# Kernel optimization log

Hardware: AMD Instinct MI355X
Metric: run time of the kernel (lower is better)

The kernel has to match this reference:

```python
import jax, jax.numpy as jnp
import numpy as np

B, N, D = 4, 1024, 512
H = 8
HD = D // H  # 64
EPS = 1e-12  # F.normalize eps


def _l2_normalize(t):
    # torch.nn.functional.normalize(p=2, dim=-1): x / max(||x||_2, eps)
    nrm = jnp.sqrt(jnp.sum(t * t, axis=-1, keepdims=True))
    return t / jnp.maximum(nrm, EPS)


def setup_inputs() -> dict:
    key = jax.random.key(0)
    ks = jax.random.split(key, 5)
    scale = 1.0 / np.sqrt(D)
    inp = {
        "x": jax.random.normal(ks[0], (B, N, D), dtype=jnp.float32),
        "Wq": jax.random.normal(ks[1], (D, D), dtype=jnp.float32) * scale,
        "Wk": jax.random.normal(ks[2], (D, D), dtype=jnp.float32) * scale,
        "Wv": jax.random.normal(ks[3], (D, D), dtype=jnp.float32) * scale,
        "Wo": jax.random.normal(ks[4], (D, D), dtype=jnp.float32) * scale,
        "bq": jnp.zeros((D,), dtype=jnp.float32),
        "bk": jnp.zeros((D,), dtype=jnp.float32),
        "bv": jnp.zeros((D,), dtype=jnp.float32),
        "bo": jnp.zeros((D,), dtype=jnp.float32),
    }
    return inp


def reference(x, Wq, Wk, Wv, Wo, bq, bk, bv, bo):
    b, n, d = x.shape
    # projections (nn.Linear: x @ W.T + b), split heads -> (b, h, n, hd)
    def split_heads(t):
        return t.reshape(b, n, H, HD).transpose(0, 2, 1, 3)

    q = split_heads(x @ Wq.T + bq)
    k = split_heads(x @ Wk.T + bk)
    v = split_heads(x @ Wv.T + bv)

    q = _l2_normalize(jax.nn.elu(q))
    k = _l2_normalize(jax.nn.elu(k))

    # causal linear attention: running prefix sum of k (outer) v states
    kv_step = jnp.einsum('bhnd,bhne->bhnde', k, v)      # (b,h,n,hd,hd)
    kv_prefix = jnp.cumsum(kv_step, axis=2)             # causal prefix state
    out = jnp.einsum('bhnd,bhnde->bhne', q, kv_prefix)  # (b,h,n,hd)

    out = out.transpose(0, 2, 1, 3).reshape(b, n, d)
    return out @ Wo.T + bo
```

## Files before the change

### kernel.cpp

```cpp
#include <hip/hip_runtime.h>
#include <cmath>

#define BB 4
#define NN 1024
#define DD 512
#define HH 8
#define HDIM 64
#define ROWS (BB * NN)
#define NCHUNK 16
#define KA 512
#define WMAT ((size_t)512 * 512)

typedef _Float16 f16;
typedef f16   f16x8 __attribute__((ext_vector_type(8)));
typedef f16   f16x4 __attribute__((ext_vector_type(4)));
typedef float f32x4 __attribute__((ext_vector_type(4)));

#define GLOAD_LDS16(g, l) \
    __builtin_amdgcn_global_load_lds((const __attribute__((address_space(1))) void*)(g), \
                                     (__attribute__((address_space(3))) void*)(l), 16, 0, 0)

__global__ __launch_bounds__(256)
void split_all(const float* __restrict__ x,
               const float* __restrict__ Wq, const float* __restrict__ Wk,
               const float* __restrict__ Wv, const float* __restrict__ Wo,
               f16* __restrict__ xa, f16* __restrict__ wa)
{
    for (int f4 = blockIdx.x * 256 + threadIdx.x; f4 < 786432; f4 += 768 * 256) {
        const float* src;
        f16* dstbase;
        int t;
        if (f4 < 524288) {
            t = f4;
            src = x;
            dstbase = xa;
        } else {
            int w = f4 - 524288;
            int m = w >> 16;
            t = w & 65535;
            src = (m == 0) ? Wq : (m == 1) ? Wk : (m == 2) ? Wv : Wo;
            dstbase = wa + (size_t)m * WMAT;
        }
        float4 v = ((const float4*)src)[t];
        int r = t >> 7;
        int c = (t & 127) * 4;
        f16x4 h;
        h[0] = (f16)v.x; h[1] = (f16)v.y; h[2] = (f16)v.z; h[3] = (f16)v.w;
        *(f16x4*)(dstbase + (size_t)r * 512 + c) = h;
    }
}

template<int OUTMODE>
__global__ __launch_bounds__(256)
void mm_f16(const f16* __restrict__ A, const f16* __restrict__ Wm,
            const float* __restrict__ b0, const float* __restrict__ b1,
            const float* __restrict__ b2,
            f16* __restrict__ qf, f16* __restrict__ kf,
            f16* __restrict__ ktb, f16* __restrict__ vtb,
            float* __restrict__ obase)
{
    constexpr int BN = (OUTMODE == 0) ? 128 : 64;
    constexpr int NW = BN / 32;
    constexpr int BR = BN / 32;

    __shared__ __align__(16) f16 As[2][128 * 64];
    __shared__ __align__(16) f16 Bs[2][BN * 64];

    const int t    = threadIdx.x;
    const int lane = t & 63;
    const int wid  = t >> 6;
    const int wr   = wid >> 1;
    const int wc   = wid & 1;
    const int l16  = lane & 15;
    const int g16  = lane >> 4;

    const int nwg = 32 * gridDim.y;
    const int lin = blockIdx.y * 32 + blockIdx.x;
    const int swz = (lin & 7) * (nwg >> 3) + (lin >> 3);
    const int bx  = swz & 31;
    const int by  = swz >> 5;

    const int r0 = bx * 128;
    const int c0 = by * BN;
    const int z  = (OUTMODE == 0) ? (c0 >> 9) : 0;
    const int cw = (OUTMODE == 0) ? (c0 & 511) : c0;

    const f16* Wz = Wm + (size_t)z * WMAT;

    auto stage = [&](int buf, int kt) {
        const int kb = kt * 64;
        #pragma unroll
        for (int i = 0; i < 4; ++i) {
            int f = i * 256 + t;
            int row = f >> 3;
            int sc  = (f & 7) ^ (row & 7);
            GLOAD_LDS16(A + (size_t)(r0 + row) * KA + kb + sc * 8, As[buf] + f * 8);
        }
        #pragma unroll
        for (int i = 0; i < BR; ++i) {
            int f = i * 256 + t;
            int row = f >> 3;
            int sc  = (f & 7) ^ (row & 7);
            GLOAD_LDS16(Wz + (size_t)(cw + row) * KA + kb + sc * 8, Bs[buf] + f * 8);
        }
    };

    f32x4 acc[4][NW] = {};

    stage(0, 0);

    for (int kt = 0; kt < 8; ++kt) {
        const int buf = kt & 1;
        if (kt < 7) {
            stage(buf ^ 1, kt + 1);
            if (OUTMODE == 0) asm volatile("s_waitcnt vmcnt(8)" ::: "memory");
            else              asm volatile("s_waitcnt vmcnt(6)" ::: "memory");
        } else {
            asm volatile("s_waitcnt vmcnt(0)" ::: "memory");
        }
        __builtin_amdgcn_s_barrier();
        __builtin_amdgcn_sched_barrier(0);

        #pragma unroll
        for (int kk = 0; kk < 2; ++kk) {
            f16x8 af[4], bfr[NW];
            #pragma unroll
            for (int mi = 0; mi < 4; ++mi) {
                int lr = wr * 64 + mi * 16 + l16;
                int sc = (kk * 4 + g16) ^ (lr & 7);
                af[mi] = *(const f16x8*)(As[buf] + lr * 64 + sc * 8);
            }
            #pragma unroll
            for (int ni = 0; ni < NW; ++ni) {
                int lr = wc * (BN / 2) + ni * 16 + l16;
                int sc = (kk * 4 + g16) ^ (lr & 7);
                bfr[ni] = *(const f16x8*)(Bs[buf] + lr * 64 + sc * 8);
            }
            #pragma unroll
            for (int mi = 0; mi < 4; ++mi)
                #pragma unroll
                for (int ni = 0; ni < NW; ++ni)
                    acc[mi][ni] = __builtin_amdgcn_mfma_f32_16x16x32_f16(af[mi], bfr[ni], acc[mi][ni], 0, 0, 0);
        }
        __builtin_amdgcn_s_barrier();
    }

    if (OUTMODE == 1) {
        #pragma unroll
        for (int mi = 0; mi < 4; ++mi)
            #pragma unroll
            for (int ni = 0; ni < NW; ++ni) {
                int cg = c0 + wc * (BN / 2) + ni * 16 + l16;
                float bv = b0[cg];
                #pragma unroll
                for (int r = 0; r < 4; ++r) {
                    int rg = r0 + wr * 64 + mi * 16 + g16 * 4 + r;
                    obase[(size_t)rg * DD + cg] = acc[mi][ni][r] + bv;
                }
            }
    } else {
        const float* bias = (z == 0) ? b0 : (z == 1) ? b1 : b2;

        #pragma unroll
        for (int mi = 0; mi < 4; ++mi)
            #pragma unroll
            for (int ni = 0; ni < NW; ++ni) {
                float bv = bias[cw + wc * 64 + ni * 16 + l16];
                #pragma unroll
                for (int r = 0; r < 4; ++r) {
                    float v = acc[mi][ni][r] + bv;
                    if (z < 2) v = (v > 0.f) ? v : expm1f(v);
                    acc[mi][ni][r] = v;
                }
            }
        if (z < 2) {
            #pragma unroll
            for (int mi = 0; mi < 4; ++mi)
                #pragma unroll
                for (int r = 0; r < 4; ++r) {
                    float ss = 0.f;
                    #pragma unroll
                    for (int ni = 0; ni < NW; ++ni) ss += acc[mi][ni][r] * acc[mi][ni][r];
                    ss += __shfl_xor(ss, 1);
                    ss += __shfl_xor(ss, 2);
                    ss += __shfl_xor(ss, 4);
                    ss += __shfl_xor(ss, 8);
                    float sc = 1.f / fmaxf(sqrtf(ss), 1e-12f);
                    #pragma unroll
                    for (int ni = 0; ni < NW; ++ni) acc[mi][ni][r] *= sc;
                }
        }

        const int h = (cw >> 6) + wc;
        const int b = r0 >> 10;

        if (z <= 1) {
            f16* plane = (z == 0) ? qf : kf;
            #pragma unroll
            for (int mi = 0; mi < 4; ++mi)
                #pragma unroll
                for (int r = 0; r < 4; ++r) {
                    int rg = r0 + wr * 64 + mi * 16 + g16 * 4 + r;
                    f16* dst = plane + ((size_t)(b * HH + h) * NN + (rg & 1023)) * HDIM;
                    #pragma unroll
                    for (int ni = 0; ni < NW; ++ni) dst[ni * 16 + l16] = (f16)acc[mi][ni][r];
                }
        }

        if (z >= 1) {
            f16* tb = (z == 1) ? ktb : vtb;
            f16* T = (wid < 2) ? (As[0] + wid * 4096) : (Bs[0] + (wid - 2) * 4096);
            #pragma unroll
            for (int mi = 0; mi < 4; ++mi)
                #pragma unroll
                for (int ni = 0; ni < NW; ++ni)
                    #pragma unroll
                    for (int r = 0; r < 4; ++r) {
                        int n_ = mi * 16 + g16 * 4 + r;
                        int d_ = ni * 16 + l16;
                        *(f16*)((char*)T + d_ * 128 + (((n_ >> 3) ^ (d_ & 7)) * 16) + (n_ & 7) * 2)
                            = (f16)acc[mi][ni][r];
                    }
            __syncthreads();
            const int n0 = (r0 & 1023) + wr * 64;
            #pragma unroll
            for (int p = 0; p < 8; ++p) {
                int d_ = p * 8 + (lane >> 3);
                int ck = lane & 7;
                f16x8 v8 = *(const f16x8*)((char*)T + d_ * 128 + ((ck ^ (d_ & 7)) * 16));
                *(f16x8*)(tb + ((size_t)(b * HH + h) * HDIM + d_) * NN + n0 + ck * 8) = v8;
            }
        }
    }
}

__global__ __launch_bounds__(256)
void state_prefix(const f16* __restrict__ ktb, const f16* __restrict__ vtb,
                  f16* __restrict__ ptb)
{
    __shared__ __align__(16) f16 Kt[2][64 * 64];
    __shared__ __align__(16) f16 Vt[2][64 * 64];
    __shared__ __align__(16) f16 PtL[16 * 64];

    const int bh = blockIdx.x;
    const int eq = blockIdx.y;
    const int t  = threadIdx.x;
    const int lane = t & 63;
    const int wid  = t >> 6;
    const int l16  = lane & 15;
    const int g16  = lane >> 4;

    auto stage = [&](int ch, int buf) {
        #pragma unroll
        for (int i = 0; i < 2; ++i) {
            int f = i * 256 + t;
            int row = f >> 3;
            int sc  = (f & 7) ^ (row & 7);
            GLOAD_LDS16(ktb + ((size_t)bh * HDIM + row) * NN + ch * 64 + sc * 8, Kt[buf] + f * 8);
            GLOAD_LDS16(vtb + ((size_t)bh * HDIM + row) * NN + ch * 64 + sc * 8, Vt[buf] + f * 8);
        }
    };

    float pref[4] = {};
    const int d = wid * 16 + l16;

    stage(0, 0);

    for (int ch = 0; ch < NCHUNK; ++ch) {
        const int buf = ch & 1;
        stage(ch < 15 ? ch + 1 : 15, buf ^ 1);

        #pragma unroll
        for (int r = 0; r < 4; ++r) {
            int e = g16 * 4 + r;
            *(f16*)((char*)PtL + e * 128 + (((d >> 3) ^ (e & 7)) * 16) + (d & 7) * 2)
                = (f16)pref[r];
        }

        asm volatile("s_waitcnt vmcnt(4)" ::: "memory");
        asm volatile("s_waitcnt lgkmcnt(0)" ::: "memory");
        __builtin_amdgcn_s_barrier();
        __builtin_amdgcn_sched_barrier(0);

        {
            f16x4 v4 = *(const f16x4*)(PtL + t * 4);
            *(f16x4*)(ptb + (size_t)(bh * NCHUNK + ch) * 4096 + eq * 1024 + t * 4) = v4;
        }

        f32x4 sacc = {};
        #pragma unroll
        for (int ks = 0; ks < 2; ++ks) {
            int ra = eq * 16 + l16;
            f16x8 av = *(const f16x8*)(Vt[buf] + ra * 64 + ((ks * 4 + g16) ^ (ra & 7)) * 8);
            int rb = wid * 16 + l16;
            f16x8 bv = *(const f16x8*)(Kt[buf] + rb * 64 + ((ks * 4 + g16) ^ (rb & 7)) * 8);
            sacc = __builtin_amdgcn_mfma_f32_16x16x32_f16(av, bv, sacc, 0, 0, 0);
        }
        #pragma unroll
        for (int r = 0; r < 4; ++r) pref[r] += sacc[r];

        __builtin_amdgcn_s_barrier();
    }
}

__global__ __launch_bounds__(256)
void attn_chunk(const f16* __restrict__ qf, const f16* __restrict__ kf,
                const f16* __restrict__ vtb, const f16* __restrict__ ptb,
                f16* __restrict__ aug)
{
    __shared__ __align__(16) f16 Qs[64 * 64];
    __shared__ __align__(16) f16 Ks[64 * 64];
    __shared__ __align__(16) f16 Vt[64 * 64];
    __shared__ __align__(16) f16 Pt[64 * 64];
    __shared__ __align__(16) f16 Ss[64 * 64];

    const int bh = blockIdx.x;
    const int ch = blockIdx.y;
    const int t  = threadIdx.x;
    const int lane = t & 63;
    const int wid  = t >> 6;
    const int wr   = wid >> 1;
    const int wc   = wid & 1;
    const int l16  = lane & 15;
    const int g16  = lane >> 4;

    #pragma unroll
    for (int i = 0; i < 2; ++i) {
        int f = i * 256 + t;
        int row = f >> 3;
        int sc  = (f & 7) ^ (row & 7);
        GLOAD_LDS16(qf  + ((size_t)bh * NN + ch * 64 + row) * HDIM + sc * 8, Qs + f * 8);
        GLOAD_LDS16(kf  + ((size_t)bh * NN + ch * 64 + row) * HDIM + sc * 8, Ks + f * 8);
        GLOAD_LDS16(vtb + ((size_t)bh * HDIM + row) * NN + ch * 64 + sc * 8, Vt + f * 8);
        GLOAD_LDS16(ptb + (size_t)(bh * NCHUNK + ch) * 4096 + f * 8, Pt + f * 8);
    }
    __syncthreads();

    f32x4 sacc[2][2] = {};
    #pragma unroll
    for (int ks = 0; ks < 2; ++ks) {
        f16x8 af[2], bfr[2];
        #pragma unroll
        for (int mi = 0; mi < 2; ++mi) {
            int row = wr * 32 + mi * 16 + l16;
            int sc  = (ks * 4 + g16) ^ (row & 7);
            af[mi] = *(const f16x8*)(Qs + row * 64 + sc * 8);
        }
        #pragma unroll
        for (int ni = 0; ni < 2; ++ni) {
            int row = wc * 32 + ni * 16 + l16;
            int sc  = (ks * 4 + g16) ^ (row & 7);
            bfr[ni] = *(const f16x8*)(Ks + row * 64 + sc * 8);
        }
        #pragma unroll
        for (int mi = 0; mi < 2; ++mi)
            #pragma unroll
            for (int ni = 0; ni < 2; ++ni)
                sacc[mi][ni] = __builtin_amdgcn_mfma_f32_16x16x32_f16(af[mi], bfr[ni], sacc[mi][ni], 0, 0, 0);
    }
    #pragma unroll
    for (int mi = 0; mi < 2; ++mi)
        #pragma unroll
        for (int ni = 0; ni < 2; ++ni)
            #pragma unroll
            for (int r = 0; r < 4; ++r) {
                int i = wr * 32 + mi * 16 + g16 * 4 + r;
                int j = wc * 32 + ni * 16 + l16;
                float v = (j <= i) ? sacc[mi][ni][r] : 0.f;
                *(f16*)((char*)Ss + i * 128 + (((j >> 3) ^ (i & 7)) * 16) + (j & 7) * 2) = (f16)v;
            }
    __syncthreads();

    f32x4 oacc[2][2] = {};
    #pragma unroll
    for (int ks = 0; ks < 2; ++ks) {
        f16x8 af[2], bfr[2];
        #pragma unroll
        for (int mi = 0; mi < 2; ++mi) {
            int row = wr * 32 + mi * 16 + l16;
            int sc  = (ks * 4 + g16) ^ (row & 7);
            af[mi] = *(const f16x8*)(Qs + row * 64 + sc * 8);
        }
        #pragma unroll
        for (int ni = 0; ni < 2; ++ni) {
            int row = wc * 32 + ni * 16 + l16;
            int sc  = (ks * 4 + g16) ^ (row & 7);
            bfr[ni] = *(const f16x8*)(Pt + row * 64 + sc * 8);
        }
        #pragma unroll
        for (int mi = 0; mi < 2; ++mi)
            #pragma unroll
            for (int ni = 0; ni < 2; ++ni)
                oacc[mi][ni] = __builtin_amdgcn_mfma_f32_16x16x32_f16(af[mi], bfr[ni], oacc[mi][ni], 0, 0, 0);
    }
    #pragma unroll
    for (int ks = 0; ks < 2; ++ks) {
        f16x8 af[2], bfr[2];
        #pragma unroll
        for (int mi = 0; mi < 2; ++mi) {
            int row = wr * 32 + mi * 16 + l16;
            int sc  = (ks * 4 + g16) ^ (row & 7);
            af[mi] = *(const f16x8*)(Ss + row * 64 + sc * 8);
        }
        #pragma unroll
        for (int ni = 0; ni < 2; ++ni) {
            int row = wc * 32 + ni * 16 + l16;
            int sc  = (ks * 4 + g16) ^ (row & 7);
            bfr[ni] = *(const f16x8*)(Vt + row * 64 + sc * 8);
        }
        #pragma unroll
        for (int mi = 0; mi < 2; ++mi)
            #pragma unroll
            for (int ni = 0; ni < 2; ++ni)
                oacc[mi][ni] = __builtin_amdgcn_mfma_f32_16x16x32_f16(af[mi], bfr[ni], oacc[mi][ni], 0, 0, 0);
    }

    const int b = bh >> 3;
    const int h = bh & 7;
    #pragma unroll
    for (int mi = 0; mi < 2; ++mi)
        #pragma unroll
        for (int ni = 0; ni < 2; ++ni)
            #pragma unroll
            for (int r = 0; r < 4; ++r) {
                int i = wr * 32 + mi * 16 + g16 * 4 + r;
                int e = wc * 32 + ni * 16 + l16;
                aug[((size_t)(b * NN + ch * 64 + i)) * KA + h * HDIM + e] = (f16)oacc[mi][ni][r];
            }
}

extern "C" void kernel_launch(void* const* d_in, const int* in_sizes, int n_in,
                              void* d_out, int out_size, void* d_ws, size_t ws_size,
                              hipStream_t stream)
{
    (void)in_sizes; (void)n_in; (void)out_size; (void)ws_size;

    const float* x  = (const float*)d_in[0];
    const float* Wq = (const float*)d_in[1];
    const float* Wk = (const float*)d_in[2];
    const float* Wv = (const float*)d_in[3];
    const float* Wo = (const float*)d_in[4];
    const float* bq = (const float*)d_in[5];
    const float* bk = (const float*)d_in[6];
    const float* bv = (const float*)d_in[7];
    const float* bo = (const float*)d_in[8];
    float* out = (float*)d_out;

    char* ws = (char*)d_ws;
    f16* qf  = (f16*)(ws);
    f16* kf  = (f16*)(ws + (size_t)4  * 1024 * 1024);
    f16* ktb = (f16*)(ws + (size_t)8  * 1024 * 1024);
    f16* vtb = (f16*)(ws + (size_t)12 * 1024 * 1024);
    f16* ptb = (f16*)(ws + (size_t)16 * 1024 * 1024);
    f16* xa  = (f16*)(ws + (size_t)20 * 1024 * 1024);
    f16* aug = (f16*)(ws + (size_t)24 * 1024 * 1024);
    f16* wa  = (f16*)(ws + (size_t)28 * 1024 * 1024);

    dim3 blk(256);

    split_all<<<dim3(768), blk, 0, stream>>>(x, Wq, Wk, Wv, Wo, xa, wa);

    mm_f16<0><<<dim3(32, 12), blk, 0, stream>>>(xa, wa, bq, bk, bv, qf, kf, ktb, vtb, nullptr);

    state_prefix<<<dim3(32, 4), blk, 0, stream>>>(ktb, vtb, ptb);
    attn_chunk<<<dim3(32, NCHUNK), blk, 0, stream>>>(qf, kf, vtb, ptb, aug);

    mm_f16<1><<<dim3(32, 8), blk, 0, stream>>>(aug, wa + (size_t)3 * WMAT, bo, nullptr, nullptr,
                                               nullptr, nullptr, nullptr, nullptr, out);
}
```

Measured before the change: 56.07 us.

## Split QKV projection and overlap Q projection with K/V state prefix kernel

The fused QKV projection is split into a K/V-only projection kernel and a combined kernel whose first 128 blocks compute the Q projection while the remaining 128 blocks run the chunked KV-state prefix scan. The Q work is independent of the prefix scan, so running both in one launch fills the device better than the small 128-block state_prefix launch did on its own. The shared GEMM body is factored into a device function using one flat LDS buffer, and the output projection becomes its own kernel. The cost is a heterogeneous kernel whose LDS footprint is sized for the GEMM path, which may limit occupancy for the prefix blocks, and the prefix blocks can become the critical path.

Result: slower. 61.16 us (+9.1%).

```diff
diff --git a/kernel.cpp b/kernel.cpp
--- a/kernel.cpp
+++ b/kernel.cpp
@@ -50,21 +50,16 @@
     }
 }
 
-template<int OUTMODE>
-__global__ __launch_bounds__(256)
-void mm_f16(const f16* __restrict__ A, const f16* __restrict__ Wm,
-            const float* __restrict__ b0, const float* __restrict__ b1,
-            const float* __restrict__ b2,
-            f16* __restrict__ qf, f16* __restrict__ kf,
-            f16* __restrict__ ktb, f16* __restrict__ vtb,
-            float* __restrict__ obase)
-{
-    constexpr int BN = (OUTMODE == 0) ? 128 : 64;
-    constexpr int NW = BN / 32;
-    constexpr int BR = BN / 32;
-
-    __shared__ __align__(16) f16 As[2][128 * 64];
-    __shared__ __align__(16) f16 Bs[2][BN * 64];
+__device__ __forceinline__
+void proj_body(const f16* __restrict__ A, const f16* __restrict__ Wz,
+               const float* __restrict__ bias, const int z,
+               const int r0, const int cw,
+               f16* __restrict__ qf, f16* __restrict__ kf,
+               f16* __restrict__ ktb, f16* __restrict__ vtb,
+               f16* lds)
+{
+    f16* As0 = lds;
+    f16* Bs0 = lds + 16384;
 
     const int t    = threadIdx.x;
     const int lane = t & 63;
@@ -74,19 +69,6 @@
     const int l16  = lane & 15;
     const int g16  = lane >> 4;
 
-    const int nwg = 32 * gridDim.y;
-    const int lin = blockIdx.y * 32 + blockIdx.x;
-    const int swz = (lin & 7) * (nwg >> 3) + (lin >> 3);
-    const int bx  = swz & 31;
-    const int by  = swz >> 5;
-
-    const int r0 = bx * 128;
-    const int c0 = by * BN;
-    const int z  = (OUTMODE == 0) ? (c0 >> 9) : 0;
-    const int cw = (OUTMODE == 0) ? (c0 & 511) : c0;
-
-    const f16* Wz = Wm + (size_t)z * WMAT;
-
     auto stage = [&](int buf, int kt) {
         const int kb = kt * 64;
         #pragma unroll
@@ -94,18 +76,18 @@
             int f = i * 256 + t;
             int row = f >> 3;
             int sc  = (f & 7) ^ (row & 7);
-            GLOAD_LDS16(A + (size_t)(r0 + row) * KA + kb + sc * 8, As[buf] + f * 8);
-        }
-        #pragma unroll
-        for (int i = 0; i < BR; ++i) {
+            GLOAD_LDS16(A + (size_t)(r0 + row) * KA + kb + sc * 8, As0 + buf * 8192 + f * 8);
+        }
+        #pragma unroll
+        for (int i = 0; i < 4; ++i) {
             int f = i * 256 + t;
             int row = f >> 3;
             int sc  = (f & 7) ^ (row & 7);
-            GLOAD_LDS16(Wz + (size_t)(cw + row) * KA + kb + sc * 8, Bs[buf] + f * 8);
+            GLOAD_LDS16(Wz + (size_t)(cw + row) * KA + kb + sc * 8, Bs0 + buf * 8192 + f * 8);
         }
     };
 
-    f32x4 acc[4][NW] = {};
+    f32x4 acc[4][4] = {};
 
     stage(0, 0);
 
@@ -113,8 +95,7 @@
         const int buf = kt & 1;
         if (kt < 7) {
             stage(buf ^ 1, kt + 1);
-            if (OUTMODE == 0) asm volatile("s_waitcnt vmcnt(8)" ::: "memory");
-            else              asm volatile("s_waitcnt vmcnt(6)" ::: "memory");
+            asm volatile("s_waitcnt vmcnt(8)" ::: "memory");
         } else {
             asm volatile("s_waitcnt vmcnt(0)" ::: "memory");
         }
@@ -123,141 +104,161 @@
 
         #pragma unroll
         for (int kk = 0; kk < 2; ++kk) {
-            f16x8 af[4], bfr[NW];
+            f16x8 af[4], bfr[4];
             #pragma unroll
             for (int mi = 0; mi < 4; ++mi) {
                 int lr = wr * 64 + mi * 16 + l16;
                 int sc = (kk * 4 + g16) ^ (lr & 7);
-                af[mi] = *(const f16x8*)(As[buf] + lr * 64 + sc * 8);
-            }
-            #pragma unroll
-            for (int ni = 0; ni < NW; ++ni) {
-                int lr = wc * (BN / 2) + ni * 16 + l16;
+                af[mi] = *(const f16x8*)(As0 + buf * 8192 + lr * 64 + sc * 8);
+            }
+            #pragma unroll
+            for (int ni = 0; ni < 4; ++ni) {
+                int lr = wc * 64 + ni * 16 + l16;
                 int sc = (kk * 4 + g16) ^ (lr & 7);
-                bfr[ni] = *(const f16x8*)(Bs[buf] + lr * 64 + sc * 8);
+                bfr[ni] = *(const f16x8*)(Bs0 + buf * 8192 + lr * 64 + sc * 8);
             }
             #pragma unroll
             for (int mi = 0; mi < 4; ++mi)
                 #pragma unroll
-                for (int ni = 0; ni < NW; ++ni)
+                for (int ni = 0; ni < 4; ++ni)
                     acc[mi][ni] = __builtin_amdgcn_mfma_f32_16x16x32_f16(af[mi], bfr[ni], acc[mi][ni], 0, 0, 0);
         }
         __builtin_amdgcn_s_barrier();
     }
 
-    if (OUTMODE == 1) {
+    #pragma unroll
+    for (int mi = 0; mi < 4; ++mi)
+        #pragma unroll
+        for (int ni = 0; ni < 4; ++ni) {
+            float bv = bias[cw + wc * 64 + ni * 16 + l16];
+            #pragma unroll
+            for (int r = 0; r < 4; ++r) {
+                float v = acc[mi][ni][r] + bv;
+                if (z < 2) v = (v > 0.f) ? v : expm1f(v);
+                acc[mi][ni][r] = v;
+            }
+        }
+    if (z < 2) {
         #pragma unroll
         for (int mi = 0; mi < 4; ++mi)
             #pragma unroll
-            for (int ni = 0; ni < NW; ++ni) {
-                int cg = c0 + wc * (BN / 2) + ni * 16 + l16;
-                float bv = b0[cg];
+            for (int r = 0; r < 4; ++r) {
+                float ss = 0.f;
+                #pragma unroll
+                for (int ni = 0; ni < 4; ++ni) ss += acc[mi][ni][r] * acc[mi][ni][r];
+                ss += __shfl_xor(ss, 1);
+                ss += __shfl_xor(ss, 2);
+                ss += __shfl_xor(ss, 4);
+                ss += __shfl_xor(ss, 8);
+                float sc = 1.f / fmaxf(sqrtf(ss), 1e-12f);
+                #pragma unroll
+                for (int ni = 0; ni < 4; ++ni) acc[mi][ni][r] *= sc;
+            }
+    }
+
+    const int h = (cw >> 6) + wc;
+    const int b = r0 >> 10;
+
+    if (z <= 1) {
+        f16* plane = (z == 0) ? qf : kf;
+        #pragma unroll
+        for (int mi = 0; mi < 4; ++mi)
+            #pragma unroll
+            for (int r = 0; r < 4; ++r) {
+                int rg = r0 + wr * 64 + mi * 16 + g16 * 4 + r;
+                f16* dst = plane + ((size_t)(b * HH + h) * NN + (rg & 1023)) * HDIM;
+                #pragma unroll
+                for (int ni = 0; ni < 4; ++ni) dst[ni * 16 + l16] = (f16)acc[mi][ni][r];
+            }
+    }
+
+    if (z >= 1) {
+        f16* tb = (z == 1) ? ktb : vtb;
+        f16* T = (wid < 2) ? (As0 + wid * 4096) : (Bs0 + (wid - 2) * 4096);
+        #pragma unroll
+        for (int mi = 0; mi < 4; ++mi)
+            #pragma unroll
+            for (int ni = 0; ni < 4; ++ni)
                 #pragma unroll
                 for (int r = 0; r < 4; ++r) {
-                    int rg = r0 + wr * 64 + mi * 16 + g16 * 4 + r;
-                    obase[(size_t)rg * DD + cg] = acc[mi][ni][r] + bv;
+                    int n_ = mi * 16 + g16 * 4 + r;
+                    int d_ = ni * 16 + l16;
+                    *(f16*)((char*)T + d_ * 128 + (((n_ >> 3) ^ (d_ & 7)) * 16) + (n_ & 7) * 2)
+                        = (f16)acc[mi][ni][r];
                 }
-            }
-    } else {
-        const float* bias = (z == 0) ? b0 : (z == 1) ? b1 : b2;
-
-        #pragma unroll
-        for (int mi = 0; mi < 4; ++mi)
-            #pragma unroll
-            for (int ni = 0; ni < NW; ++ni) {
-                float bv = bias[cw + wc * 64 + ni * 16 + l16];
-                #pragma unroll
-                for (int r = 0; r < 4; ++r) {
-                    float v = acc[mi][ni][r] + bv;
-                    if (z < 2) v = (v > 0.f) ? v : expm1f(v);
-                    acc[mi][ni][r] = v;
-                }
-            }
-        if (z < 2) {
-            #pragma unroll
-            for (int mi = 0; mi < 4; ++mi)
-                #pragma unroll
-                for (int r = 0; r < 4; ++r) {
-                    float ss = 0.f;
-                    #pragma unroll
-                    for (int ni = 0; ni < NW; ++ni) ss += acc[mi][ni][r] * acc[mi][ni][r];
-                    ss += __shfl_xor(ss, 1);
-                    ss += __shfl_xor(ss, 2);
-                    ss += __shfl_xor(ss, 4);
-                    ss += __shfl_xor(ss, 8);
-                    float sc = 1.f / fmaxf(sqrtf(ss), 1e-12f);
-                    #pragma unroll
-                    for (int ni = 0; ni < NW; ++ni) acc[mi][ni][r] *= sc;
-                }
-        }
-
-        const int h = (cw >> 6) + wc;
-        const int b = r0 >> 10;
-
-        if (z <= 1) {
-            f16* plane = (z == 0) ? qf : kf;
-            #pragma unroll
-            for (int mi = 0; mi < 4; ++mi)
-                #pragma unroll
-                for (int r = 0; r < 4; ++r) {
-                    int rg = r0 + wr * 64 + mi * 16 + g16 * 4 + r;
-                    f16* dst = plane + ((size_t)(b * HH + h) * NN + (rg & 1023)) * HDIM;
-                    #pragma unroll
-                    for (int ni = 0; ni < NW; ++ni) dst[ni * 16 + l16] = (f16)acc[mi][ni][r];
-                }
-        }
-
-        if (z >= 1) {
-            f16* tb = (z == 1) ? ktb : vtb;
-            f16* T = (wid < 2) ? (As[0] + wid * 4096) : (Bs[0] + (wid - 2) * 4096);
-            #pragma unroll
-            for (int mi = 0; mi < 4; ++mi)
-                #pragma unroll
-                for (int ni = 0; ni < NW; ++ni)
-                    #pragma unroll
-                    for (int r = 0; r < 4; ++r) {
-                        int n_ = mi * 16 + g16 * 4 + r;
-                        int d_ = ni * 16 + l16;
-                        *(f16*)((char*)T + d_ * 128 + (((n_ >> 3) ^ (d_ & 7)) * 16) + (n_ & 7) * 2)
-                            = (f16)acc[mi][ni][r];
-                    }
-            __syncthreads();
-            const int n0 = (r0 & 1023) + wr * 64;
-            #pragma unroll
-            for (int p = 0; p < 8; ++p) {
-                int d_ = p * 8 + (lane >> 3);
-                int ck = lane & 7;
-                f16x8 v8 = *(const f16x8*)((char*)T + d_ * 128 + ((ck ^ (d_ & 7)) * 16));
-                *(f16x8*)(tb + ((size_t)(b * HH + h) * HDIM + d_) * NN + n0 + ck * 8) = v8;
-            }
+        __syncthreads();
+        const int n0 = (r0 & 1023) + wr * 64;
+        #pragma unroll
+        for (int p = 0; p < 8; ++p) {
+            int d_ = p * 8 + (lane >> 3);
+            int ck = lane & 7;
+            f16x8 v8 = *(const f16x8*)((char*)T + d_ * 128 + ((ck ^ (d_ & 7)) * 16));
+            *(f16x8*)(tb + ((size_t)(b * HH + h) * HDIM + d_) * NN + n0 + ck * 8) = v8;
         }
     }
 }
 
 __global__ __launch_bounds__(256)
-void state_prefix(const f16* __restrict__ ktb, const f16* __restrict__ vtb,
-                  f16* __restrict__ ptb)
-{
-    __shared__ __align__(16) f16 Kt[2][64 * 64];
-    __shared__ __align__(16) f16 Vt[2][64 * 64];
-    __shared__ __align__(16) f16 PtL[16 * 64];
-
-    const int bh = blockIdx.x;
-    const int eq = blockIdx.y;
-    const int t  = threadIdx.x;
+void mm_kv(const f16* __restrict__ xa, const f16* __restrict__ wa,
+           const float* __restrict__ bk, const float* __restrict__ bv,
+           f16* __restrict__ kf, f16* __restrict__ ktb, f16* __restrict__ vtb)
+{
+    __shared__ __align__(16) f16 LB[32768];
+
+    const int lin = blockIdx.x;
+    const int swz = (lin & 7) * 32 + (lin >> 3);
+    const int bx  = swz & 31;
+    const int by  = swz >> 5;
+
+    const int r0 = bx * 128;
+    const int c0 = by * 128;
+    const int z  = 1 + (c0 >> 9);
+    const int cw = c0 & 511;
+
+    proj_body(xa, wa + (size_t)z * WMAT, (z == 1) ? bk : bv, z,
+              r0, cw, nullptr, kf, ktb, vtb, LB);
+}
+
+__global__ __launch_bounds__(256)
+void q_and_state(const f16* __restrict__ xa, const f16* __restrict__ wa,
+                 const float* __restrict__ bq,
+                 const f16* __restrict__ ktb, const f16* __restrict__ vtb,
+                 f16* __restrict__ qf, f16* __restrict__ ptb)
+{
+    __shared__ __align__(16) f16 LB[32768];
+
+    const int t    = threadIdx.x;
     const int lane = t & 63;
     const int wid  = t >> 6;
     const int l16  = lane & 15;
     const int g16  = lane >> 4;
 
+    if (blockIdx.x < 128) {
+        const int lin = blockIdx.x;
+        const int swz = (lin & 7) * 16 + (lin >> 3);
+        const int bx  = swz & 31;
+        const int by  = swz >> 5;
+        proj_body(xa, wa, bq, 0, bx * 128, by * 128,
+                  qf, nullptr, nullptr, nullptr, LB);
+        return;
+    }
+
+    const int idx = blockIdx.x - 128;
+    const int bh = idx >> 2;
+    const int eq = idx & 3;
+
+    f16* Kt0 = LB;
+    f16* Vt0 = LB + 8192;
+    f16* PtL = LB + 16384;
+
     auto stage = [&](int ch, int buf) {
         #pragma unroll
         for (int i = 0; i < 2; ++i) {
             int f = i * 256 + t;
             int row = f >> 3;
             int sc  = (f & 7) ^ (row & 7);
-            GLOAD_LDS16(ktb + ((size_t)bh * HDIM + row) * NN + ch * 64 + sc * 8, Kt[buf] + f * 8);
-            GLOAD_LDS16(vtb + ((size_t)bh * HDIM + row) * NN + ch * 64 + sc * 8, Vt[buf] + f * 8);
+            GLOAD_LDS16(ktb + ((size_t)bh * HDIM + row) * NN + ch * 64 + sc * 8, Kt0 + buf * 4096 + f * 8);
+            GLOAD_LDS16(vtb + ((size_t)bh * HDIM + row) * NN + ch * 64 + sc * 8, Vt0 + buf * 4096 + f * 8);
         }
     };
 
@@ -291,9 +292,9 @@
         #pragma unroll
         for (int ks = 0; ks < 2; ++ks) {
             int ra = eq * 16 + l16;
-            f16x8 av = *(const f16x8*)(Vt[buf] + ra * 64 + ((ks * 4 + g16) ^ (ra & 7)) * 8);
+            f16x8 av = *(const f16x8*)(Vt0 + buf * 4096 + ra * 64 + ((ks * 4 + g16) ^ (ra & 7)) * 8);
             int rb = wid * 16 + l16;
-            f16x8 bv = *(const f16x8*)(Kt[buf] + rb * 64 + ((ks * 4 + g16) ^ (rb & 7)) * 8);
+            f16x8 bv = *(const f16x8*)(Kt0 + buf * 4096 + rb * 64 + ((ks * 4 + g16) ^ (rb & 7)) * 8);
             sacc = __builtin_amdgcn_mfma_f32_16x16x32_f16(av, bv, sacc, 0, 0, 0);
         }
         #pragma unroll
@@ -427,6 +428,101 @@
                 int e = wc * 32 + ni * 16 + l16;
                 aug[((size_t)(b * NN + ch * 64 + i)) * KA + h * HDIM + e] = (f16)oacc[mi][ni][r];
             }
+}
+
+__global__ __launch_bounds__(256)
+void mm_out(const f16* __restrict__ A, const f16* __restrict__ Wz,
+            const float* __restrict__ bo, float* __restrict__ out)
+{
+    __shared__ __align__(16) f16 As[2][128 * 64];
+    __shared__ __align__(16) f16 Bs[2][64 * 64];
+
+    const int t    = threadIdx.x;
+    const int lane = t & 63;
+    const int wid  = t >> 6;
+    const int wr   = wid >> 1;
+    const int wc   = wid & 1;
+    const int l16  = lane & 15;
+    const int g16  = lane >> 4;
+
+    const int nwg = 32 * gridDim.y;
+    const int lin = blockIdx.y * 32 + blockIdx.x;
+    const int swz = (lin & 7) * (nwg >> 3) + (lin >> 3);
+    const int bx  = swz & 31;
+    const int by  = swz >> 5;
+
+    const int r0 = bx * 128;
+    const int c0 = by * 64;
+
+    auto stage = [&](int buf, int kt) {
+        const int kb = kt * 64;
+        #pragma unroll
+        for (int i = 0; i < 4; ++i) {
+            int f = i * 256 + t;
+            int row = f >> 3;
+            int sc  = (f & 7) ^ (row & 7);
+            GLOAD_LDS16(A + (size_t)(r0 + row) * KA + kb + sc * 8, As[buf] + f * 8);
+        }
+        #pragma unroll
+        for (int i = 0; i < 2; ++i) {
+            int f = i * 256 + t;
+            int row = f >> 3;
+            int sc  = (f & 7) ^ (row & 7);
+            GLOAD_LDS16(Wz + (size_t)(c0 + row) * KA + kb + sc * 8, Bs[buf] + f * 8);
+        }
+    };
+
+    f32x4 acc[4][2] = {};
+
+    stage(0, 0);
+
+    for (int kt = 0; kt < 8; ++kt) {
+        const int buf = kt & 1;
+        if (kt < 7) {
+            stage(buf ^ 1, kt + 1);
+            asm volatile("s_waitcnt vmcnt(6)" ::: "memory");
+        } else {
+            asm volatile("s_waitcnt vmcnt(0)" ::: "memory");
+        }
+        __builtin_amdgcn_s_barrier();
+        __builtin_amdgcn_sched_barrier(0);
+
+        #pragma unroll
+        for (int kk = 0; kk < 2; ++kk) {
+            f16x8 af[4], bfr[2];
+            #pragma unroll
+            for (int mi = 0; mi < 4; ++mi) {
+                int lr = wr * 64 + mi * 16 + l16;
+                int sc = (kk * 4 + g16) ^ (lr & 7);
+                af[mi] = *(const f16x8*)(As[buf] + lr * 64 + sc * 8);
+            }
+            #pragma unroll
+            for (int ni = 0; ni < 2; ++ni) {
+                int lr = wc * 32 + ni * 16 + l16;
+                int sc = (kk * 4 + g16) ^ (lr & 7);
+                bfr[ni] = *(const f16x8*)(Bs[buf] + lr * 64 + sc * 8);
+            }
+            #pragma unroll
+            for (int mi = 0; mi < 4; ++mi)
+                #pragma unroll
+                for (int ni = 0; ni < 2; ++ni)
+                    acc[mi][ni] = __builtin_amdgcn_mfma_f32_16x16x32_f16(af[mi], bfr[ni], acc[mi][ni], 0, 0, 0);
+        }
+        __builtin_amdgcn_s_barrier();
+    }
+
+    #pragma unroll
+    for (int mi = 0; mi < 4; ++mi)
+        #pragma unroll
+        for (int ni = 0; ni < 2; ++ni) {
+            int cg = c0 + wc * 32 + ni * 16 + l16;
+            float bv = bo[cg];
+            #pragma unroll
+            for (int r = 0; r < 4; ++r) {
+                int rg = r0 + wr * 64 + mi * 16 + g16 * 4 + r;
+                out[(size_t)rg * DD + cg] = acc[mi][ni][r] + bv;
+            }
+        }
 }
 
 extern "C" void kernel_launch(void* const* d_in, const int* in_sizes, int n_in,
@@ -460,11 +556,11 @@
 
     split_all<<<dim3(768), blk, 0, stream>>>(x, Wq, Wk, Wv, Wo, xa, wa);
 
-    mm_f16<0><<<dim3(32, 12), blk, 0, stream>>>(xa, wa, bq, bk, bv, qf, kf, ktb, vtb, nullptr);
-
-    state_prefix<<<dim3(32, 4), blk, 0, stream>>>(ktb, vtb, ptb);
+    mm_kv<<<dim3(256), blk, 0, stream>>>(xa, wa, bk, bv, kf, ktb, vtb);
+
+    q_and_state<<<dim3(256), blk, 0, stream>>>(xa, wa, bq, ktb, vtb, qf, ptb);
+
     attn_chunk<<<dim3(32, NCHUNK), blk, 0, stream>>>(qf, kf, vtb, ptb, aug);
 
-    mm_f16<1><<<dim3(32, 8), blk, 0, stream>>>(aug, wa + (size_t)3 * WMAT, bo, nullptr, nullptr,
-                                               nullptr, nullptr, nullptr, nullptr, out);
-}
+    mm_out<<<dim3(32, 8), blk, 0, stream>>>(aug, wa + (size_t)3 * WMAT, bo, out);
+}
```
